# Kernel tuning notes

Hardware: AMD Instinct MI355X
Metric: run time of the kernel (lower is better)

## Reference

```python
import jax, jax.numpy as jnp
import numpy as np

EPS = 1e-7  # torchvision distance_box_iou_loss eps


def cxcywh_to_xyxy(b):
    cx, cy, w, h = b[..., 0], b[..., 1], b[..., 2], b[..., 3]
    return jnp.stack([cx - w / 2, cy - h / 2, cx + w / 2, cy + h / 2], axis=-1)


def iou_and_diou(b1, b2):
    # b1, b2: broadcastable [..., 4] in xyxy. Returns (plain iou, diou loss).
    x1, y1, x2, y2 = b1[..., 0], b1[..., 1], b1[..., 2], b1[..., 3]
    xg1, yg1, xg2, yg2 = b2[..., 0], b2[..., 1], b2[..., 2], b2[..., 3]
    xi1 = jnp.maximum(x1, xg1); yi1 = jnp.maximum(y1, yg1)
    xi2 = jnp.minimum(x2, xg2); yi2 = jnp.minimum(y2, yg2)
    inter = jnp.clip(xi2 - xi1, 0.0) * jnp.clip(yi2 - yi1, 0.0)
    union = (x2 - x1) * (y2 - y1) + (xg2 - xg1) * (yg2 - yg1) - inter
    iou = inter / union                 # ops.box_iou: no eps
    iou_e = inter / (union + EPS)       # distance_box_iou_loss: eps
    xc1 = jnp.minimum(x1, xg1); yc1 = jnp.minimum(y1, yg1)
    xc2 = jnp.maximum(x2, xg2); yc2 = jnp.maximum(y2, yg2)
    diag = (xc2 - xc1) ** 2 + (yc2 - yc1) ** 2 + EPS
    dist = ((x1 + x2 - xg1 - xg2) * 0.5) ** 2 + ((y1 + y2 - yg1 - yg2) * 0.5) ** 2
    return iou, 1.0 - iou_e + dist / diag


def bce(p, t):
    # torch binary_cross_entropy clamps log terms at -100
    lnp = jnp.maximum(jnp.log(p), -100.0)
    ln1 = jnp.maximum(jnp.log(1.0 - p), -100.0)
    return -(t * lnp + (1.0 - t) * ln1)


def hungarian(cost):
    # O(n^3) Hungarian (Kuhn-Munkres with potentials) on a square matrix.
    # Returns col assignment per row (row_ind = arange(n)). Matches scipy
    # linear_sum_assignment for square inputs.
    n = cost.shape[0]
    INF = np.inf
    u = np.zeros(n + 1); v = np.zeros(n + 1)
    p = np.zeros(n + 1, dtype=np.int64)
    way = np.zeros(n + 1, dtype=np.int64)
    for i in range(1, n + 1):
        p[0] = i
        j0 = 0
        minv = np.full(n + 1, INF)
        used = np.zeros(n + 1, dtype=bool)
        while True:
            used[j0] = True
            i0 = p[j0]
            cur = cost[i0 - 1] - u[i0] - v[1:]
            free = ~used[1:]
            upd = free & (cur < minv[1:])
            minv[1:] = np.where(upd, cur, minv[1:])
            way[1:] = np.where(upd, j0, way[1:])
            masked = np.where(free, minv[1:], INF)
            j1 = int(np.argmin(masked)) + 1
            delta = masked[j1 - 1]
            uidx = np.nonzero(used)[0]
            u[p[uidx]] += delta
            v[uidx] -= delta
            minv[1:] = np.where(free, minv[1:] - delta, minv[1:])
            j0 = j1
            if p[j0] == 0:
                break
        while j0:
            j1 = way[j0]
            p[j0] = p[j1]
            j0 = j1
    col_of_row = np.empty(n, dtype=np.int64)
    col_of_row[p[1:] - 1] = np.arange(n)
    return col_of_row


def build_cost_and_match(p, bbox_pred, labels_target, bbox_target):
    # Fused, fully vectorized replacement of the original O(N*M) python loop.
    pb = cxcywh_to_xyxy(bbox_pred)   # [B,N,4]
    tb = cxcywh_to_xyxy(bbox_target)  # [B,M,4]
    _, diou_pair = iou_and_diou(pb[:, :, None, :], tb[:, None, :, :])  # [B,N,M]
    # original uses reduction='mean' BCE/L1 over the batch -> batch-constant [N,M]
    label_cost = bce(p[:, :, None], labels_target[:, None, :]).mean(axis=0)  # [N,M]
    l1_cost = jnp.abs(bbox_pred[:, :, None, :] - bbox_target[:, None, :, :]).mean(axis=(0, 3))
    cost = diou_pair + label_cost[None] + l1_cost[None]  # [B,N,M]
    cost_np = np.asarray(jax.device_get(cost), dtype=np.float64)
    cols = np.stack([hungarian(cost_np[b]) for b in range(cost_np.shape[0])])
    return jnp.asarray(cols)  # [B,N]


def matched_losses(labels_pred, bbox_pred, labels_target, bbox_target, cols):
    p = jax.nn.sigmoid(labels_pred[..., 0])  # [B,N]
    B = p.shape[0]
    bi = jnp.arange(B)[:, None]
    # square matching: row indices are arange(N), only targets get permuted
    t_m = labels_target[bi, cols]   # [B,N]
    bt_m = bbox_target[bi, cols]    # [B,N,4]
    w = jax.lax.stop_gradient((t_m == 1.0).astype(p.dtype))  # positives mask
    iou_e, diou_e = iou_and_diou(cxcywh_to_xyxy(bbox_pred), cxcywh_to_xyxy(bt_m))
    wsum = w.sum()
    diou_loss = (diou_e * w).sum() / wsum
    iou = (iou_e * w).sum() / wsum
    label_loss = bce(p, t_m).mean()
    bbox_loss = (jnp.abs(bbox_pred - bt_m) * w[..., None]).sum() / (wsum * 4.0)
    return diou_loss + label_loss + bbox_loss, iou


def setup_inputs() -> dict:
    key = jax.random.key(0)
    k1, k2, k3, k4 = jax.random.split(key, 4)
    B, N, M = 64, 256, 256
    labels_pred = jax.random.normal(k1, (B, N, 1), dtype=jnp.float32)
    # cxcywh boxes in (0.05, 0.95) so areas/unions are strictly positive
    bbox_pred = jax.random.uniform(k2, (B, N, 4), dtype=jnp.float32) * 0.9 + 0.05
    labels_target = jax.random.randint(k3, (B, M), 0, 2).astype(jnp.float32)
    bbox_target = jax.random.uniform(k4, (B, M, 4), dtype=jnp.float32) * 0.9 + 0.05
    return {"labels_pred": labels_pred, "bbox_pred": bbox_pred,
            "labels_target": labels_target, "bbox_target": bbox_target}


def reference(labels_pred, bbox_pred, labels_target, bbox_target):
    p = jax.nn.sigmoid(labels_pred[..., 0])
    cols = build_cost_and_match(p, bbox_pred, labels_target, bbox_target)
    total_loss, iou = matched_losses(labels_pred, bbox_pred, labels_target, bbox_target, cols)
    return total_loss, iou
```

## Files before the change

### kernel.cpp

```cpp
#include <hip/hip_runtime.h>
#include <math.h>

#define BB 64
#define NN 256
#define MM 256
#define EPSF 1e-7f
#define ROWS_LDS 157


__device__ __forceinline__ void iou_diou(const float4 pb, const float4 tb,
                                         float& iou, float& diou) {
    float x1 = pb.x - pb.z * 0.5f, y1 = pb.y - pb.w * 0.5f;
    float x2 = pb.x + pb.z * 0.5f, y2 = pb.y + pb.w * 0.5f;
    float xg1 = tb.x - tb.z * 0.5f, yg1 = tb.y - tb.w * 0.5f;
    float xg2 = tb.x + tb.z * 0.5f, yg2 = tb.y + tb.w * 0.5f;
    float xi1 = fmaxf(x1, xg1), yi1 = fmaxf(y1, yg1);
    float xi2 = fminf(x2, xg2), yi2 = fminf(y2, yg2);
    float inter = fmaxf(xi2 - xi1, 0.f) * fmaxf(yi2 - yi1, 0.f);
    float uni = (x2 - x1) * (y2 - y1) + (xg2 - xg1) * (yg2 - yg1) - inter;
    iou = inter / uni;
    float iou_e = inter / (uni + EPSF);
    float xc1 = fminf(x1, xg1), yc1 = fminf(y1, yg1);
    float xc2 = fmaxf(x2, xg2), yc2 = fmaxf(y2, yg2);
    float dx = xc2 - xc1, dy = yc2 - yc1;
    float diag = dx * dx + dy * dy + EPSF;
    float ex = (x1 + x2 - xg1 - xg2) * 0.5f;
    float ey = (y1 + y2 - yg1 - yg2) * 0.5f;
    float dist = ex * ex + ey * ey;
    diou = 1.f - iou_e + dist / diag;
}

__device__ __forceinline__ unsigned long long dkey(double d, int j) {
    unsigned long long b = (unsigned long long)__double_as_longlong(d);
    b ^= (b >> 63) ? 0xFFFFFFFFFFFFFFFFULL : 0x8000000000000000ULL;
    return (b & ~511ULL) | (unsigned long long)j;
}
__device__ __forceinline__ double unkey(unsigned long long k) {
    unsigned long long b = k & ~511ULL;
    b ^= (b & 0x8000000000000000ULL) ? 0x8000000000000000ULL : 0xFFFFFFFFFFFFFFFFULL;
    return __longlong_as_double((long long)b);
}

#define SEL4I(s, a0, a1, a2, a3) ((s) == 0 ? (a0) : (s) == 1 ? (a1) : (s) == 2 ? (a2) : (a3))
#define SEL4D(s, a0, a1, a2, a3) ((s) == 0 ? (a0) : (s) == 1 ? (a1) : (s) == 2 ? (a2) : (a3))

__device__ __forceinline__ double readlane_d(double v, int lane) {
    unsigned long long b = (unsigned long long)__double_as_longlong(v);
    int lo = __builtin_amdgcn_readlane((int)(unsigned int)b, lane);
    int hi = __builtin_amdgcn_readlane((int)(unsigned int)(b >> 32), lane);
    return __longlong_as_double((long long)(((unsigned long long)(unsigned int)hi << 32) |
                                            (unsigned long long)(unsigned int)lo));
}

#define RED_DPP_K(CTRL)                                                                     \
    do {                                                                                    \
        int lo_ = (int)(unsigned int)ka, hi_ = (int)(unsigned int)(ka >> 32);               \
        int nlo_ = __builtin_amdgcn_update_dpp(lo_, lo_, CTRL, 0xF, 0xF, false);            \
        int nhi_ = __builtin_amdgcn_update_dpp(hi_, hi_, CTRL, 0xF, 0xF, false);            \
        unsigned long long ok_ = ((unsigned long long)(unsigned int)nhi_ << 32) |           \
                                 (unsigned long long)(unsigned int)nlo_;                    \
        if (ok_ < ka) ka = ok_;                                                             \
    } while (0)

#define RED_ALL()                                                                           \
    do {                                                                                    \
        RED_DPP_K(0x111); RED_DPP_K(0x112); RED_DPP_K(0x114); RED_DPP_K(0x118);             \
        RED_DPP_K(0x142); RED_DPP_K(0x143);                                                 \
        unsigned int klo_ = (unsigned int)__builtin_amdgcn_readlane((int)(unsigned int)ka, 63); \
        unsigned int khi_ = (unsigned int)__builtin_amdgcn_readlane((int)(unsigned int)(ka >> 32), 63); \
        ka = ((unsigned long long)khi_ << 32) | klo_;                                       \
    } while (0)

__global__ __launch_bounds__(256) void k_prep(const float* __restrict__ lp,
                                              float* __restrict__ A,
                                              float* __restrict__ C) {
    int idx = blockIdx.x * 256 + threadIdx.x;
    float x = lp[idx];
    float p = 1.f / (1.f + expf(-x));
    A[idx] = -fmaxf(logf(p), -100.f);
    C[idx] = -fmaxf(logf(1.f - p), -100.f);
}

__global__ __launch_bounds__(256) void k_nm(const float* __restrict__ A,
                                            const float* __restrict__ C,
                                            const float* __restrict__ bp,
                                            const float* __restrict__ bt,
                                            const float* __restrict__ lt,
                                            float* __restrict__ lc,
                                            float* __restrict__ l1c) {
    int n = blockIdx.x, m = threadIdx.x;
    float sl = 0.f, s1 = 0.f;
    for (int b = 0; b < BB; ++b) {
        float a = A[b * NN + n];
        float c = C[b * NN + n];
        float t = lt[b * MM + m];
        sl += t * a + (1.f - t) * c;
        float4 P = *reinterpret_cast<const float4*>(bp + ((size_t)b * NN + n) * 4);
        float4 T = *reinterpret_cast<const float4*>(bt + ((size_t)b * MM + m) * 4);
        s1 += fabsf(P.x - T.x) + fabsf(P.y - T.y) + fabsf(P.z - T.z) + fabsf(P.w - T.w);
    }
    lc[n * MM + m]  = sl * (1.f / 64.f);
    l1c[n * MM + m] = s1 * (1.f / 256.f);
}

__global__ __launch_bounds__(256) void k_cost(const float* __restrict__ bp,
                                              const float* __restrict__ bt,
                                              const float* __restrict__ lc,
                                              const float* __restrict__ l1c,
                                              float* __restrict__ cost) {
    int bn = blockIdx.x;
    int b = bn >> 8, n = bn & 255;
    int m = threadIdx.x;
    float4 P = *reinterpret_cast<const float4*>(bp + ((size_t)bn) * 4);
    float4 T = *reinterpret_cast<const float4*>(bt + ((size_t)b * MM + m) * 4);
    float iou, diou;
    iou_diou(P, T, iou, diou);
    cost[((size_t)bn << 8) + m] = diou + lc[(n << 8) + m] + l1c[(n << 8) + m];
}

__global__ __launch_bounds__(64) void k_hungarian(const float* __restrict__ cost,
                                                  int* __restrict__ cols) {
    const int b = blockIdx.x;
    const int lane = threadIdx.x;
    const float* Cm = cost + (size_t)b * NN * MM;
    const unsigned long long MAXK = 0xFFFFFFFFFFFFFFFFULL;
    const double INFD = __builtin_inf();

    __shared__ float ldsC[ROWS_LDS * MM];
    __shared__ int jofrow[NN + 1];
    __shared__ int matches[NN + 1];
    for (int r = lane; r <= NN; r += 64) { jofrow[r] = 0x7fffffff; matches[r] = 0; }
    __syncthreads();

    float cm0 = __builtin_inff(), cm1 = cm0, cm2 = cm0, cm3 = cm0;
    int rm0 = 0, rm1 = 0, rm2 = 0, rm3 = 0;
    #pragma unroll 4
    for (int i = 0; i < NN; ++i) {
        float4 cr = *reinterpret_cast<const float4*>(Cm + (size_t)i * MM + 4 * lane);
        if (i < ROWS_LDS) *reinterpret_cast<float4*>(&ldsC[i * MM + 4 * lane]) = cr;
        if (cr.x < cm0) { cm0 = cr.x; rm0 = i; }
        if (cr.y < cm1) { cm1 = cr.y; rm1 = i; }
        if (cr.z < cm2) { cm2 = cr.z; rm2 = i; }
        if (cr.w < cm3) { cm3 = cr.w; rm3 = i; }
    }
    atomicMin(&jofrow[rm0 + 1], 4 * lane + 1);
    atomicMin(&jofrow[rm1 + 1], 4 * lane + 2);
    atomicMin(&jofrow[rm2 + 1], 4 * lane + 3);
    atomicMin(&jofrow[rm3 + 1], 4 * lane + 4);
    atomicAdd(&matches[rm0 + 1], 1);
    atomicAdd(&matches[rm1 + 1], 1);
    atomicAdd(&matches[rm2 + 1], 1);
    atomicAdd(&matches[rm3 + 1], 1);
    __syncthreads();

    double vj0 = cm0, vj1 = cm1, vj2 = cm2, vj3 = cm3;
    double up0 = 0.0, up1 = 0.0, up2 = 0.0, up3 = 0.0;
    int pj0_ = (jofrow[rm0 + 1] == 4 * lane + 1) ? rm0 + 1 : 0;
    int pj1_ = (jofrow[rm1 + 1] == 4 * lane + 2) ? rm1 + 1 : 0;
    int pj2_ = (jofrow[rm2 + 1] == 4 * lane + 3) ? rm2 + 1 : 0;
    int pj3_ = (jofrow[rm3 + 1] == 4 * lane + 4) ? rm3 + 1 : 0;
    int wy0 = 0, wy1 = 0, wy2 = 0, wy3 = 0;

    unsigned long long am0 = __ballot(jofrow[1 + lane]       != 0x7fffffff);
    unsigned long long am1 = __ballot(jofrow[1 + 64 + lane]  != 0x7fffffff);
    unsigned long long am2 = __ballot(jofrow[1 + 128 + lane] != 0x7fffffff);
    unsigned long long am3 = __ballot(jofrow[1 + 192 + lane] != 0x7fffffff);

    for (int i = 1; i <= NN; ++i) {
        if (matches[i] != 1) continue;
        int j1 = jofrow[i];
        int o = (j1 - 1) >> 2, s = (j1 - 1) & 3;
        float4 cr;
        if (i - 1 < ROWS_LDS)
            cr = *reinterpret_cast<const float4*>(&ldsC[(i - 1) * MM + 4 * lane]);
        else
            cr = *reinterpret_cast<const float4*>(Cm + (size_t)(i - 1) * MM + 4 * lane);
        double h0 = (double)cr.x - vj0;
        double h1 = (double)cr.y - vj1;
        double h2 = (double)cr.z - vj2;
        double h3 = (double)cr.w - vj3;
        if (lane == o) {
            if (s == 0) h0 = INFD; else if (s == 1) h1 = INFD;
            else if (s == 2) h2 = INFD; else h3 = INFD;
        }
        double hm = fmin(fmin(h0, h1), fmin(h2, h3));
        unsigned long long ka = (unsigned long long)__double_as_longlong(hm);
        RED_ALL();
        double m = __longlong_as_double((long long)ka);
        if (lane == o) {
            if (s == 0)      { vj0 -= m; up0 += m; }
            else if (s == 1) { vj1 -= m; up1 += m; }
            else if (s == 2) { vj2 -= m; up2 += m; }
            else             { vj3 -= m; up3 += m; }
        }
    }

    for (int i = 1; i <= NN; ++i) {
        unsigned long long amv = (i <= 64) ? am0 : (i <= 128) ? am1 : (i <= 192) ? am2 : am3;
        if ((amv >> ((i - 1) & 63)) & 1ULL) continue;
        float4 cr;
        if (i - 1 < ROWS_LDS)
            cr = *reinterpret_cast<const float4*>(&ldsC[(i - 1) * MM + 4 * lane]);
        else
            cr = *reinterpret_cast<const float4*>(Cm + (size_t)(i - 1) * MM + 4 * lane);
        double h0 = (double)cr.x - vj0;
        double h1 = (double)cr.y - vj1;
        double h2 = (double)cr.z - vj2;
        double h3 = (double)cr.w - vj3;
        unsigned long long k0 = dkey(h0, 4 * lane + 1);
        unsigned long long k1 = dkey(h1, 4 * lane + 2);
        unsigned long long k2 = dkey(h2, 4 * lane + 3);
        unsigned long long k3 = dkey(h3, 4 * lane + 4);
        unsigned long long ea = k1 < k0 ? k1 : k0;
        unsigned long long eb = k3 < k2 ? k3 : k2;
        unsigned long long ka = eb < ea ? eb : ea;
        RED_ALL();
        int j1 = (int)(ka & 511ULL);
        int o1 = (j1 - 1) >> 2, s1 = (j1 - 1) & 3;
        int pcur = __builtin_amdgcn_readlane(SEL4I(s1, pj0_, pj1_, pj2_, pj3_), o1);
        if (pcur == 0) {
            double u_i = unkey(ka);
            if (lane == o1) {
                if (s1 == 0)      { pj0_ = i; up0 = u_i; }
                else if (s1 == 1) { pj1_ = i; up1 = u_i; }
                else if (s1 == 2) { pj2_ = i; up2 = u_i; }
                else              { pj3_ = i; up3 = u_i; }
            }
            unsigned long long bit = 1ULL << ((i - 1) & 63);
            if (i <= 64) am0 |= bit; else if (i <= 128) am1 |= bit;
            else if (i <= 192) am2 |= bit; else am3 |= bit;
        }
    }

    for (int i = 1; i <= NN; ++i) {
        unsigned long long amv = (i <= 64) ? am0 : (i <= 128) ? am1 : (i <= 192) ? am2 : am3;
        if ((amv >> ((i - 1) & 63)) & 1ULL) continue;

        double u_i = 0.0;
        double mv0 = INFD, mv1 = INFD, mv2 = INFD, mv3 = INFD;
        int used4 = 0;
        int j0 = 0;
        int i0 = i;
        double ui0 = 0.0;

        for (int it = 0; it <= NN; ++it) {
            double uv0 = ui0 + vj0, uv1 = ui0 + vj1, uv2 = ui0 + vj2, uv3 = ui0 + vj3;
            float4 cr;
            if (i0 - 1 < ROWS_LDS)
                cr = *reinterpret_cast<const float4*>(&ldsC[(i0 - 1) * MM + 4 * lane]);
            else
                cr = *reinterpret_cast<const float4*>(Cm + (size_t)(i0 - 1) * MM + 4 * lane);

            if (!(used4 & 1)) { double cur = (double)cr.x - uv0; if (cur < mv0) { mv0 = cur; wy0 = j0; } }
            if (!(used4 & 2)) { double cur = (double)cr.y - uv1; if (cur < mv1) { mv1 = cur; wy1 = j0; } }
            if (!(used4 & 4)) { double cur = (double)cr.z - uv2; if (cur < mv2) { mv2 = cur; wy2 = j0; } }
            if (!(used4 & 8)) { double cur = (double)cr.w - uv3; if (cur < mv3) { mv3 = cur; wy3 = j0; } }

            unsigned long long k0 = (used4 & 1) ? MAXK : dkey(mv0, 4 * lane + 1);
            unsigned long long k1 = (used4 & 2) ? MAXK : dkey(mv1, 4 * lane + 2);
            unsigned long long k2 = (used4 & 4) ? MAXK : dkey(mv2, 4 * lane + 3);
            unsigned long long k3 = (used4 & 8) ? MAXK : dkey(mv3, 4 * lane + 4);

            unsigned long long ea = k1 < k0 ? k1 : k0;
            unsigned long long eb = k3 < k2 ? k3 : k2;
            unsigned long long ka = eb < ea ? eb : ea;

            RED_ALL();

            double delta = unkey(ka);
            int j1 = (int)(ka & 511ULL);
            int o1 = (j1 - 1) >> 2, s1 = (j1 - 1) & 3;
            int pa = __builtin_amdgcn_readlane(SEL4I(s1, pj0_, pj1_, pj2_, pj3_), o1);
            double ua = readlane_d(SEL4D(s1, up0, up1, up2, up3), o1);

            u_i += delta;
            if (used4 & 1) { up0 += delta; vj0 -= delta; } else { mv0 -= delta; }
            if (used4 & 2) { up1 += delta; vj1 -= delta; } else { mv1 -= delta; }
            if (used4 & 4) { up2 += delta; vj2 -= delta; } else { mv2 -= delta; }
            if (used4 & 8) { up3 += delta; vj3 -= delta; } else { mv3 -= delta; }

            j0 = j1;
            if (pa == 0) break;
            int ci = j1 - 1;
            if ((ci >> 2) == lane) used4 |= 1 << (ci & 3);
            i0 = pa;
            ui0 = ua;
        }

        int jj = j0;
        while (jj) {
            int o = (jj - 1) >> 2, s = (jj - 1) & 3;
            int wv = SEL4I(s, wy0, wy1, wy2, wy3);
            int jn = __builtin_amdgcn_readlane(wv, o);
            int pn; double un;
            if (jn == 0) { pn = i; un = u_i; }
            else {
                int o2 = (jn - 1) >> 2, s2 = (jn - 1) & 3;
                int pv = SEL4I(s2, pj0_, pj1_, pj2_, pj3_);
                double uv = SEL4D(s2, up0, up1, up2, up3);
                pn = __builtin_amdgcn_readlane(pv, o2);
                un = readlane_d(uv, o2);
            }
            if (lane == o) {
                if (s == 0)      { pj0_ = pn; up0 = un; }
                else if (s == 1) { pj1_ = pn; up1 = un; }
                else if (s == 2) { pj2_ = pn; up2 = un; }
                else             { pj3_ = pn; up3 = un; }
            }
            jj = jn;
        }
    }

    cols[b * NN + (pj0_ - 1)] = 4 * lane + 0;
    cols[b * NN + (pj1_ - 1)] = 4 * lane + 1;
    cols[b * NN + (pj2_ - 1)] = 4 * lane + 2;
    cols[b * NN + (pj3_ - 1)] = 4 * lane + 3;
}

__global__ __launch_bounds__(256) void k_loss(const float* __restrict__ lp,
                                              const float* __restrict__ bp,
                                              const float* __restrict__ lt,
                                              const float* __restrict__ bt,
                                              const int* __restrict__ cols,
                                              float* __restrict__ partials) {
    int b = blockIdx.x, n = threadIdx.x;
    int col = cols[b * NN + n];
    float x = lp[b * NN + n];
    float pp = 1.f / (1.f + expf(-x));
    float t = lt[b * MM + col];
    float4 P = *reinterpret_cast<const float4*>(bp + ((size_t)b * NN + n) * 4);
    float4 T = *reinterpret_cast<const float4*>(bt + ((size_t)b * MM + col) * 4);
    float w = (t == 1.f) ? 1.f : 0.f;
    float iou, diou;
    iou_diou(P, T, iou, diou);
    float bce = -(t * fmaxf(logf(pp), -100.f) + (1.f - t) * fmaxf(logf(1.f - pp), -100.f));
    float l1 = fabsf(P.x - T.x) + fabsf(P.y - T.y) + fabsf(P.z - T.z) + fabsf(P.w - T.w);

    float v0 = w, v1 = diou * w, v2 = iou * w, v3 = bce, v4 = l1 * w;
    #pragma unroll
    for (int mm = 1; mm < 64; mm <<= 1) {
        v0 += __shfl_xor(v0, mm); v1 += __shfl_xor(v1, mm);
        v2 += __shfl_xor(v2, mm); v3 += __shfl_xor(v3, mm);
        v4 += __shfl_xor(v4, mm);
    }
    __shared__ float red[4][5];
    int wid = n >> 6, lane = n & 63;
    if (lane == 0) { red[wid][0] = v0; red[wid][1] = v1; red[wid][2] = v2; red[wid][3] = v3; red[wid][4] = v4; }
    __syncthreads();
    if (n == 0) {
        float s0 = red[0][0] + red[1][0] + red[2][0] + red[3][0];
        float s1 = red[0][1] + red[1][1] + red[2][1] + red[3][1];
        float s2 = red[0][2] + red[1][2] + red[2][2] + red[3][2];
        float s3 = red[0][3] + red[1][3] + red[2][3] + red[3][3];
        float s4 = red[0][4] + red[1][4] + red[2][4] + red[3][4];
        partials[b * 8 + 0] = s0; partials[b * 8 + 1] = s1; partials[b * 8 + 2] = s2;
        partials[b * 8 + 3] = s3; partials[b * 8 + 4] = s4;
    }
}

__global__ __launch_bounds__(64) void k_final(const float* __restrict__ partials,
                                              float* __restrict__ out) {
    int t = threadIdx.x;
    float v0 = partials[t * 8 + 0], v1 = partials[t * 8 + 1], v2 = partials[t * 8 + 2];
    float v3 = partials[t * 8 + 3], v4 = partials[t * 8 + 4];
    #pragma unroll
    for (int mm = 1; mm < 64; mm <<= 1) {
        v0 += __shfl_xor(v0, mm); v1 += __shfl_xor(v1, mm);
        v2 += __shfl_xor(v2, mm); v3 += __shfl_xor(v3, mm);
        v4 += __shfl_xor(v4, mm);
    }
    if (t == 0) {
        float wsum = v0;
        float diou_loss = v1 / wsum;
        float iou = v2 / wsum;
        float label_loss = v3 * (1.f / (64.f * 256.f));
        float bbox_loss = v4 / (wsum * 4.f);
        out[0] = diou_loss + label_loss + bbox_loss;
        out[1] = iou;
    }
}

extern "C" void kernel_launch(void* const* d_in, const int* in_sizes, int n_in,
                              void* d_out, int out_size, void* d_ws, size_t ws_size,
                              hipStream_t stream) {
    const float* labels_pred   = (const float*)d_in[0];
    const float* bbox_pred     = (const float*)d_in[1];
    const float* labels_target = (const float*)d_in[2];
    const float* bbox_target   = (const float*)d_in[3];
    float* out = (float*)d_out;

    float* A    = (float*)d_ws;
    float* C    = A + BB * NN;
    float* lc   = C + BB * NN;
    float* l1c  = lc + NN * MM;
    float* cost = l1c + NN * MM;
    int*   cols = (int*)(cost + (size_t)BB * NN * MM);
    float* partials = (float*)(cols + BB * NN);

    k_prep<<<BB * NN / 256, 256, 0, stream>>>(labels_pred, A, C);
    k_nm<<<NN, MM, 0, stream>>>(A, C, bbox_pred, bbox_target, labels_target, lc, l1c);
    k_cost<<<BB * NN, MM, 0, stream>>>(bbox_pred, bbox_target, lc, l1c, cost);
    k_hungarian<<<BB, 64, 0, stream>>>(cost, cols);
    k_loss<<<BB, NN, 0, stream>>>(labels_pred, bbox_pred, labels_target, bbox_target, cols, partials);
    k_final<<<1, 64, 0, stream>>>(partials, out);
}
```

Before: 2.811 ms.

## Add row-reduction potentials before column reduction in Hungarian initialization

Computes a per-row minimum via DPP wave reduction while loading the cost matrix and stores it as an initial row potential u in LDS. Column reductions, the reduction-transfer and augmenting-row-reduction phases then work on row-reduced costs, aiming for tighter initial duals and fewer or shorter augmenting-path searches in the main Hungarian loop. This adds a wave reduction per row during loading, moves the column-min tracking to doubles, and shrinks the LDS cost cache by one row to make room for the potentials array.

```diff
diff --git a/kernel.cpp b/kernel.cpp
--- a/kernel.cpp
+++ b/kernel.cpp
@@ -5,7 +5,7 @@
 #define NN 256
 #define MM 256
 #define EPSF 1e-7f
-#define ROWS_LDS 157
+#define ROWS_LDS 156
 
 
 __device__ __forceinline__ void iou_diou(const float4 pb, const float4 tb,
@@ -71,6 +71,18 @@
         ka = ((unsigned long long)khi_ << 32) | klo_;                                       \
     } while (0)
 
+#define RED_U32_STEP(CTRL)                                                                  \
+    do {                                                                                    \
+        unsigned int n_ = (unsigned int)__builtin_amdgcn_update_dpp((int)kb, (int)kb, CTRL, 0xF, 0xF, false); \
+        if (n_ < kb) kb = n_;                                                               \
+    } while (0)
+#define RED_U32_ALL()                                                                       \
+    do {                                                                                    \
+        RED_U32_STEP(0x111); RED_U32_STEP(0x112); RED_U32_STEP(0x114); RED_U32_STEP(0x118); \
+        RED_U32_STEP(0x142); RED_U32_STEP(0x143);                                           \
+        kb = (unsigned int)__builtin_amdgcn_readlane((int)kb, 63);                          \
+    } while (0)
+
 __global__ __launch_bounds__(256) void k_prep(const float* __restrict__ lp,
                                               float* __restrict__ A,
                                               float* __restrict__ C) {
@@ -127,21 +139,31 @@
     const double INFD = __builtin_inf();
 
     __shared__ float ldsC[ROWS_LDS * MM];
+    __shared__ float ldsU[NN];
     __shared__ int jofrow[NN + 1];
     __shared__ int matches[NN + 1];
     for (int r = lane; r <= NN; r += 64) { jofrow[r] = 0x7fffffff; matches[r] = 0; }
     __syncthreads();
 
-    float cm0 = __builtin_inff(), cm1 = cm0, cm2 = cm0, cm3 = cm0;
+    double cm0 = INFD, cm1 = INFD, cm2 = INFD, cm3 = INFD;
     int rm0 = 0, rm1 = 0, rm2 = 0, rm3 = 0;
-    #pragma unroll 4
     for (int i = 0; i < NN; ++i) {
         float4 cr = *reinterpret_cast<const float4*>(Cm + (size_t)i * MM + 4 * lane);
         if (i < ROWS_LDS) *reinterpret_cast<float4*>(&ldsC[i * MM + 4 * lane]) = cr;
-        if (cr.x < cm0) { cm0 = cr.x; rm0 = i; }
-        if (cr.y < cm1) { cm1 = cr.y; rm1 = i; }
-        if (cr.z < cm2) { cm2 = cr.z; rm2 = i; }
-        if (cr.w < cm3) { cm3 = cr.w; rm3 = i; }
+        float rl = fminf(fminf(cr.x, cr.y), fminf(cr.z, cr.w));
+        unsigned int kb = __float_as_uint(rl);
+        RED_U32_ALL();
+        float u0i = __uint_as_float(kb);
+        if (lane == 0) ldsU[i] = u0i;
+        double du = (double)u0i;
+        double h0 = (double)cr.x - du;
+        double h1 = (double)cr.y - du;
+        double h2 = (double)cr.z - du;
+        double h3 = (double)cr.w - du;
+        if (h0 < cm0) { cm0 = h0; rm0 = i; }
+        if (h1 < cm1) { cm1 = h1; rm1 = i; }
+        if (h2 < cm2) { cm2 = h2; rm2 = i; }
+        if (h3 < cm3) { cm3 = h3; rm3 = i; }
     }
     atomicMin(&jofrow[rm0 + 1], 4 * lane + 1);
     atomicMin(&jofrow[rm1 + 1], 4 * lane + 2);
@@ -154,11 +176,14 @@
     __syncthreads();
 
     double vj0 = cm0, vj1 = cm1, vj2 = cm2, vj3 = cm3;
-    double up0 = 0.0, up1 = 0.0, up2 = 0.0, up3 = 0.0;
     int pj0_ = (jofrow[rm0 + 1] == 4 * lane + 1) ? rm0 + 1 : 0;
     int pj1_ = (jofrow[rm1 + 1] == 4 * lane + 2) ? rm1 + 1 : 0;
     int pj2_ = (jofrow[rm2 + 1] == 4 * lane + 3) ? rm2 + 1 : 0;
     int pj3_ = (jofrow[rm3 + 1] == 4 * lane + 4) ? rm3 + 1 : 0;
+    double up0 = pj0_ ? (double)ldsU[pj0_ - 1] : 0.0;
+    double up1 = pj1_ ? (double)ldsU[pj1_ - 1] : 0.0;
+    double up2 = pj2_ ? (double)ldsU[pj2_ - 1] : 0.0;
+    double up3 = pj3_ ? (double)ldsU[pj3_ - 1] : 0.0;
     int wy0 = 0, wy1 = 0, wy2 = 0, wy3 = 0;
 
     unsigned long long am0 = __ballot(jofrow[1 + lane]       != 0x7fffffff);
@@ -175,10 +200,11 @@
             cr = *reinterpret_cast<const float4*>(&ldsC[(i - 1) * MM + 4 * lane]);
         else
             cr = *reinterpret_cast<const float4*>(Cm + (size_t)(i - 1) * MM + 4 * lane);
-        double h0 = (double)cr.x - vj0;
-        double h1 = (double)cr.y - vj1;
-        double h2 = (double)cr.z - vj2;
-        double h3 = (double)cr.w - vj3;
+        double du = (double)ldsU[i - 1];
+        double h0 = ((double)cr.x - du) - vj0;
+        double h1 = ((double)cr.y - du) - vj1;
+        double h2 = ((double)cr.z - du) - vj2;
+        double h3 = ((double)cr.w - du) - vj3;
         if (lane == o) {
             if (s == 0) h0 = INFD; else if (s == 1) h1 = INFD;
             else if (s == 2) h2 = INFD; else h3 = INFD;
@@ -203,10 +229,11 @@
             cr = *reinterpret_cast<const float4*>(&ldsC[(i - 1) * MM + 4 * lane]);
         else
             cr = *reinterpret_cast<const float4*>(Cm + (size_t)(i - 1) * MM + 4 * lane);
-        double h0 = (double)cr.x - vj0;
-        double h1 = (double)cr.y - vj1;
-        double h2 = (double)cr.z - vj2;
-        double h3 = (double)cr.w - vj3;
+        double du = (double)ldsU[i - 1];
+        double h0 = ((double)cr.x - du) - vj0;
+        double h1 = ((double)cr.y - du) - vj1;
+        double h2 = ((double)cr.z - du) - vj2;
+        double h3 = ((double)cr.w - du) - vj3;
         unsigned long long k0 = dkey(h0, 4 * lane + 1);
         unsigned long long k1 = dkey(h1, 4 * lane + 2);
         unsigned long long k2 = dkey(h2, 4 * lane + 3);
@@ -219,7 +246,7 @@
         int o1 = (j1 - 1) >> 2, s1 = (j1 - 1) & 3;
         int pcur = __builtin_amdgcn_readlane(SEL4I(s1, pj0_, pj1_, pj2_, pj3_), o1);
         if (pcur == 0) {
-            double u_i = unkey(ka);
+            double u_i = du + unkey(ka);
             if (lane == o1) {
                 if (s1 == 0)      { pj0_ = i; up0 = u_i; }
                 else if (s1 == 1) { pj1_ = i; up1 = u_i; }
@@ -236,12 +263,12 @@
         unsigned long long amv = (i <= 64) ? am0 : (i <= 128) ? am1 : (i <= 192) ? am2 : am3;
         if ((amv >> ((i - 1) & 63)) & 1ULL) continue;
 
-        double u_i = 0.0;
+        double u_i = (double)ldsU[i - 1];
         double mv0 = INFD, mv1 = INFD, mv2 = INFD, mv3 = INFD;
         int used4 = 0;
         int j0 = 0;
         int i0 = i;
-        double ui0 = 0.0;
+        double ui0 = u_i;
 
         for (int it = 0; it <= NN; ++it) {
             double uv0 = ui0 + vj0, uv1 = ui0 + vj1, uv2 = ui0 + vj2, uv3 = ui0 + vj3;
```

New measurement: 2.454 ms (median of 2 runs). 12.7% less time.
